# Performance work log

Hardware: AMD Instinct MI355X
Metric: run time of the kernel (lower is better)

The kernel has to match this reference:

```python
import jax, jax.numpy as jnp
import numpy as np

B_LARGE, B_SMALL = 256, 256
R_LARGE, R_SMALL = 64, 16
N_LARGE, N_SMALL = 128, 128
D = 4096


def setup_inputs() -> dict:
    key = jax.random.key(0)
    k1, k2, k3, k4, k5 = jax.random.split(key, 5)
    x = jax.random.normal(k1, (B_LARGE + B_SMALL, 1, D), dtype=jnp.float16)
    wids_large = jax.random.randint(k2, (B_LARGE,), 0, N_LARGE, dtype=jnp.int32)
    wids_small = jax.random.randint(k3, (B_SMALL,), 0, N_SMALL, dtype=jnp.int32)
    lora_A_large = (jax.random.normal(k4, (N_LARGE, D, R_LARGE), dtype=jnp.float16) * jnp.float16(0.02))
    lora_A_small = (jax.random.normal(k5, (N_SMALL, D, R_SMALL), dtype=jnp.float16) * jnp.float16(0.02))
    return {"x": x, "wids_large": wids_large, "wids_small": wids_small,
            "lora_A_large": lora_A_large, "lora_A_small": lora_A_small}


def reference(x, wids_large, wids_small, lora_A_large, lora_A_small):
    # split batch into large / small adapter groups
    x_l = x[:B_LARGE]          # [Bl, 1, D]
    x_s = x[B_LARGE:]          # [Bs, 1, D]
    # gather per-sample adapter matrices, then batched matmul (BGMV pattern)
    A_l = lora_A_large[wids_large]   # [Bl, D, r_large]
    A_s = lora_A_small[wids_small]   # [Bs, D, r_small]
    y_large = jnp.einsum('bsd,bdr->bsr', x_l, A_l)  # [Bl, 1, r_large]
    y_small = jnp.einsum('bsd,bdr->bsr', x_s, A_s)  # [Bs, 1, r_small]
    return (y_large, y_small)
```

## Files before the change

### kernel.cpp

```cpp
#include <hip/hip_runtime.h>

#define NDIM 4096
#define B_LG 256
#define B_SM 256
#define N_WID 128
#define R_LG 64
#define R_SM 16
#define BLOCK 512
#define MAXB 256
#define PF 8
#define OUT_SIZE (B_LG * R_LG + B_SM * R_SM)

typedef float floatv4 __attribute__((ext_vector_type(4)));

#define WS_CNT_L 0
#define WS_CNT_S 128
#define WS_BKT_L 256
#define WS_BKT_S (256 + N_WID * MAXB)

__global__ __launch_bounds__(BLOCK)
void setup_kernel(const int* __restrict__ wids_l,
                  const int* __restrict__ wids_s,
                  int* __restrict__ ws,
                  float* __restrict__ out)
{
    __shared__ int cl[N_WID], cs[N_WID];
    const int t = threadIdx.x;
    if (t < N_WID) { cl[t] = 0; cs[t] = 0; }
    __syncthreads();
    if (t < B_LG) {
        const int w = wids_l[t];
        const int s = atomicAdd(&cl[w], 1);
        ws[WS_BKT_L + w * MAXB + s] = t;
    } else if (t < B_LG + B_SM) {
        const int b = t - B_LG;
        const int w = wids_s[b];
        const int s = atomicAdd(&cs[w], 1);
        ws[WS_BKT_S + w * MAXB + s] = b;
    }
    __syncthreads();
    if (t < N_WID) { ws[WS_CNT_L + t] = cl[t]; ws[WS_CNT_S + t] = cs[t]; }
    for (int i = t; i < OUT_SIZE; i += BLOCK) out[i] = 0.0f;
}

template<int R, int M, int DCH>
__device__ __forceinline__ void gemv_chunk(
    const float* __restrict__ x,
    const float* __restrict__ Ab,
    float* __restrict__ outb,
    const int* __restrict__ batches,
    int d0,
    float* __restrict__ xs,
    float* __restrict__ red)
{
    constexpr int LPR  = R / 4;
    constexpr int ROWS = BLOCK / LPR;
    constexpr int IT   = DCH / ROWS;
    constexpr int NG   = IT / PF;

    const int t = threadIdx.x;

    int rows[M];
#pragma unroll
    for (int m = 0; m < M; ++m) rows[m] = batches[m];

    __syncthreads();
#pragma unroll
    for (int m = 0; m < M; ++m)
        for (int i = t; i < DCH / 4; i += BLOCK)
            reinterpret_cast<float4*>(xs + m * DCH)[i] =
                reinterpret_cast<const float4*>(x + (size_t)rows[m] * NDIM + d0)[i];
    __syncthreads();

    const int d_sub  = t / LPR;
    const int r_base = (t % LPR) * 4;
    const float* Abt = Ab + ((size_t)d0 + d_sub) * R + r_base;

    float acc[M][4];
#pragma unroll
    for (int m = 0; m < M; ++m)
#pragma unroll
        for (int j = 0; j < 4; ++j) acc[m][j] = 0.0f;

#pragma unroll
    for (int g = 0; g < NG; ++g) {
        floatv4 buf[PF];
#pragma unroll
        for (int p = 0; p < PF; ++p)
            buf[p] = __builtin_nontemporal_load(
                reinterpret_cast<const floatv4*>(Abt + (size_t)(g * PF + p) * ROWS * R));
#pragma unroll
        for (int p = 0; p < PF; ++p) {
            const int d = (g * PF + p) * ROWS + d_sub;
#pragma unroll
            for (int m = 0; m < M; ++m) {
                const float xv = xs[m * DCH + d];
                acc[m][0] = fmaf(xv, buf[p].x, acc[m][0]);
                acc[m][1] = fmaf(xv, buf[p].y, acc[m][1]);
                acc[m][2] = fmaf(xv, buf[p].z, acc[m][2]);
                acc[m][3] = fmaf(xv, buf[p].w, acc[m][3]);
            }
        }
    }

    const int wave = t >> 6;
    const int lane = t & 63;
#pragma unroll
    for (int m = 0; m < M; ++m)
#pragma unroll
        for (int off = 32; off >= LPR; off >>= 1)
#pragma unroll
            for (int j = 0; j < 4; ++j)
                acc[m][j] += __shfl_down(acc[m][j], off, 64);

#pragma unroll
    for (int m = 0; m < M; ++m) {
        __syncthreads();
        if (lane < LPR)
#pragma unroll
            for (int j = 0; j < 4; ++j) red[(wave * 16 + lane) * 4 + j] = acc[m][j];
        __syncthreads();
        if (t < R) {
            const int rl = t / 4, j = t % 4;
            float v = 0.0f;
#pragma unroll
            for (int w = 0; w < 8; ++w) v += red[(w * 16 + rl) * 4 + j];
            atomicAdd(outb + (size_t)rows[m] * R + t, v);
        }
    }
}

template<int R, int DCH, int MAXM>
__device__ __forceinline__ void run_wid_chunk(
    const float* x, const float* Ab, float* outb,
    const int* bucket, int count, int d0,
    float* xs, float* red)
{
    for (int g = 0; g < count; g += MAXM) {
        const int Mi = min(MAXM, count - g);
        const int* b = bucket + g;
        if (Mi == 1)      gemv_chunk<R, 1, DCH>(x, Ab, outb, b, d0, xs, red);
        else if (Mi == 2) gemv_chunk<R, 2, DCH>(x, Ab, outb, b, d0, xs, red);
        else if (Mi == 3) gemv_chunk<R, 3, DCH>(x, Ab, outb, b, d0, xs, red);
        else {
            if constexpr (MAXM > 3) {
                if (Mi == 4)      gemv_chunk<R, 4, DCH>(x, Ab, outb, b, d0, xs, red);
                else if (Mi == 5) gemv_chunk<R, 5, DCH>(x, Ab, outb, b, d0, xs, red);
                else              gemv_chunk<R, 6, DCH>(x, Ab, outb, b, d0, xs, red);
            }
        }
    }
}

__global__ __launch_bounds__(BLOCK, 4)
void SequentialLoraA_kernel(const float* __restrict__ x,
                            const float* __restrict__ Al,
                            const float* __restrict__ As,
                            float* __restrict__ out,
                            const int* __restrict__ ws)
{
    __shared__ float xs[6 * 1024];
    __shared__ float red[8 * 16 * 4];

    const int blk = blockIdx.x;
    if (blk < 4 * N_WID) {
        const int wid = blk >> 2;
        const int d0  = (blk & 3) * 1024;
        run_wid_chunk<R_LG, 1024, 6>(x,
                                     Al + (size_t)wid * NDIM * R_LG,
                                     out,
                                     ws + WS_BKT_L + wid * MAXB,
                                     ws[WS_CNT_L + wid], d0,
                                     xs, red);
    } else {
        const int b2  = blk - 4 * N_WID;
        const int wid = b2 >> 1;
        const int d0  = (b2 & 1) * 2048;
        run_wid_chunk<R_SM, 2048, 3>(x + (size_t)B_LG * NDIM,
                                     As + (size_t)wid * NDIM * R_SM,
                                     out + (size_t)B_LG * R_LG,
                                     ws + WS_BKT_S + wid * MAXB,
                                     ws[WS_CNT_S + wid], d0,
                                     xs, red);
    }
}

extern "C" void kernel_launch(void* const* d_in, const int* in_sizes, int n_in,
                              void* d_out, int out_size, void* d_ws, size_t ws_size,
                              hipStream_t stream) {
    const float* x      = (const float*)d_in[0];
    const int*   wids_l = (const int*)d_in[1];
    const int*   wids_s = (const int*)d_in[2];
    const float* Al     = (const float*)d_in[3];
    const float* As     = (const float*)d_in[4];
    float* out = (float*)d_out;
    int*   ws  = (int*)d_ws;

    setup_kernel<<<1, BLOCK, 0, stream>>>(wids_l, wids_s, ws, out);
    SequentialLoraA_kernel<<<6 * N_WID, BLOCK, 0, stream>>>(x, Al, As, out, ws);
}
```

Baseline: 223.7 us.

## Replace static per-adapter grid with dynamic work queue over finer D-chunks

The setup kernel now builds a flat list of work items, one per (adapter, group of up to 6 samples, D-chunk), and the main kernel pulls items from it through an atomic ticket in a persistent-style loop over 1024 blocks. D-chunks shrink (512 for large rank, 1024 for small rank), so there are more, smaller items and less imbalance from adapters that have many samples. The cost is one atomic per item, extra barriers, more atomicAdd partial-sum traffic on the output, and some repeated reads of x.

```diff
diff --git a/kernel.cpp b/kernel.cpp
--- a/kernel.cpp
+++ b/kernel.cpp
@@ -8,15 +8,25 @@
 #define R_SM 16
 #define BLOCK 512
 #define MAXB 256
+#define MAXM 6
 #define PF 8
 #define OUT_SIZE (B_LG * R_LG + B_SM * R_SM)
 
+#define DCH_LG 512
+#define DCH_SM 1024
+#define NCH_LG (NDIM / DCH_LG)
+#define NCH_SM (NDIM / DCH_SM)
+
 typedef float floatv4 __attribute__((ext_vector_type(4)));
 
-#define WS_CNT_L 0
-#define WS_CNT_S 128
-#define WS_BKT_L 256
-#define WS_BKT_S (256 + N_WID * MAXB)
+#define WS_CNT_L  0
+#define WS_CNT_S  128
+#define WS_NWORK  256
+#define WS_TICKET 260
+#define WS_BKT_L  512
+#define WS_BKT_S  (WS_BKT_L + N_WID * MAXB)
+#define WS_WORK   (WS_BKT_S + N_WID * MAXB)
+#define MAX_WORK  4096
 
 __global__ __launch_bounds__(BLOCK)
 void setup_kernel(const int* __restrict__ wids_l,
@@ -25,8 +35,10 @@
                   float* __restrict__ out)
 {
     __shared__ int cl[N_WID], cs[N_WID];
+    __shared__ int nwork;
     const int t = threadIdx.x;
     if (t < N_WID) { cl[t] = 0; cs[t] = 0; }
+    if (t == 0) nwork = 0;
     __syncthreads();
     if (t < B_LG) {
         const int w = wids_l[t];
@@ -39,7 +51,30 @@
         ws[WS_BKT_S + w * MAXB + s] = b;
     }
     __syncthreads();
-    if (t < N_WID) { ws[WS_CNT_L + t] = cl[t]; ws[WS_CNT_S + t] = cs[t]; }
+    if (t < N_WID) {
+        ws[WS_CNT_L + t] = cl[t];
+        ws[WS_CNT_S + t] = cs[t];
+        int cnt = cl[t];
+        for (int g = 0; g < cnt; g += MAXM) {
+            const int Mi   = min(MAXM, cnt - g);
+            const int base = atomicAdd(&nwork, NCH_LG);
+            for (int c = 0; c < NCH_LG; ++c) {
+                ws[WS_WORK + 2 * (base + c)]     = (t << 8) | c;
+                ws[WS_WORK + 2 * (base + c) + 1] = (g << 8) | Mi;
+            }
+        }
+        cnt = cs[t];
+        for (int g = 0; g < cnt; g += MAXM) {
+            const int Mi   = min(MAXM, cnt - g);
+            const int base = atomicAdd(&nwork, NCH_SM);
+            for (int c = 0; c < NCH_SM; ++c) {
+                ws[WS_WORK + 2 * (base + c)]     = (1 << 30) | (t << 8) | c;
+                ws[WS_WORK + 2 * (base + c) + 1] = (g << 8) | Mi;
+            }
+        }
+    }
+    __syncthreads();
+    if (t == 0) { ws[WS_NWORK] = nwork; ws[WS_TICKET] = 0; }
     for (int i = t; i < OUT_SIZE; i += BLOCK) out[i] = 0.0f;
 }
 
@@ -64,7 +99,6 @@
 #pragma unroll
     for (int m = 0; m < M; ++m) rows[m] = batches[m];
 
-    __syncthreads();
 #pragma unroll
     for (int m = 0; m < M; ++m)
         for (int i = t; i < DCH / 4; i += BLOCK)
@@ -130,58 +164,60 @@
     }
 }
 
-template<int R, int DCH, int MAXM>
-__device__ __forceinline__ void run_wid_chunk(
-    const float* x, const float* Ab, float* outb,
-    const int* bucket, int count, int d0,
-    float* xs, float* red)
-{
-    for (int g = 0; g < count; g += MAXM) {
-        const int Mi = min(MAXM, count - g);
-        const int* b = bucket + g;
-        if (Mi == 1)      gemv_chunk<R, 1, DCH>(x, Ab, outb, b, d0, xs, red);
-        else if (Mi == 2) gemv_chunk<R, 2, DCH>(x, Ab, outb, b, d0, xs, red);
-        else if (Mi == 3) gemv_chunk<R, 3, DCH>(x, Ab, outb, b, d0, xs, red);
-        else {
-            if constexpr (MAXM > 3) {
-                if (Mi == 4)      gemv_chunk<R, 4, DCH>(x, Ab, outb, b, d0, xs, red);
-                else if (Mi == 5) gemv_chunk<R, 5, DCH>(x, Ab, outb, b, d0, xs, red);
-                else              gemv_chunk<R, 6, DCH>(x, Ab, outb, b, d0, xs, red);
-            }
-        }
-    }
-}
-
 __global__ __launch_bounds__(BLOCK, 4)
 void SequentialLoraA_kernel(const float* __restrict__ x,
                             const float* __restrict__ Al,
                             const float* __restrict__ As,
                             float* __restrict__ out,
-                            const int* __restrict__ ws)
+                            int* __restrict__ ws)
 {
-    __shared__ float xs[6 * 1024];
+    __shared__ float xs[MAXM * DCH_SM];
     __shared__ float red[8 * 16 * 4];
-
-    const int blk = blockIdx.x;
-    if (blk < 4 * N_WID) {
-        const int wid = blk >> 2;
-        const int d0  = (blk & 3) * 1024;
-        run_wid_chunk<R_LG, 1024, 6>(x,
-                                     Al + (size_t)wid * NDIM * R_LG,
-                                     out,
-                                     ws + WS_BKT_L + wid * MAXB,
-                                     ws[WS_CNT_L + wid], d0,
-                                     xs, red);
-    } else {
-        const int b2  = blk - 4 * N_WID;
-        const int wid = b2 >> 1;
-        const int d0  = (b2 & 1) * 2048;
-        run_wid_chunk<R_SM, 2048, 3>(x + (size_t)B_LG * NDIM,
-                                     As + (size_t)wid * NDIM * R_SM,
-                                     out + (size_t)B_LG * R_LG,
-                                     ws + WS_BKT_S + wid * MAXB,
-                                     ws[WS_CNT_S + wid], d0,
-                                     xs, red);
+    __shared__ int s_item;
+
+    const int t  = threadIdx.x;
+    const int nw = ws[WS_NWORK];
+
+    for (;;) {
+        __syncthreads();
+        if (t == 0) s_item = atomicAdd(ws + WS_TICKET, 1);
+        __syncthreads();
+        const int it = s_item;
+        if (it >= nw) return;
+
+        const int a   = ws[WS_WORK + 2 * it];
+        const int b   = ws[WS_WORK + 2 * it + 1];
+        const int wid = (a >> 8) & 0x7f;
+        const int Mi  = b & 0xff;
+        const int gs  = b >> 8;
+
+        if (a & (1 << 30)) {
+            const int d0 = (a & 0xff) * DCH_SM;
+            const float* xb  = x + (size_t)B_LG * NDIM;
+            const float* Ab  = As + (size_t)wid * NDIM * R_SM;
+            float*       ob  = out + (size_t)B_LG * R_LG;
+            const int*   bkt = ws + WS_BKT_S + wid * MAXB + gs;
+            switch (Mi) {
+              case 1: gemv_chunk<R_SM, 1, DCH_SM>(xb, Ab, ob, bkt, d0, xs, red); break;
+              case 2: gemv_chunk<R_SM, 2, DCH_SM>(xb, Ab, ob, bkt, d0, xs, red); break;
+              case 3: gemv_chunk<R_SM, 3, DCH_SM>(xb, Ab, ob, bkt, d0, xs, red); break;
+              case 4: gemv_chunk<R_SM, 4, DCH_SM>(xb, Ab, ob, bkt, d0, xs, red); break;
+              case 5: gemv_chunk<R_SM, 5, DCH_SM>(xb, Ab, ob, bkt, d0, xs, red); break;
+              default: gemv_chunk<R_SM, 6, DCH_SM>(xb, Ab, ob, bkt, d0, xs, red); break;
+            }
+        } else {
+            const int d0 = (a & 0xff) * DCH_LG;
+            const float* Ab  = Al + (size_t)wid * NDIM * R_LG;
+            const int*   bkt = ws + WS_BKT_L + wid * MAXB + gs;
+            switch (Mi) {
+              case 1: gemv_chunk<R_LG, 1, DCH_LG>(x, Ab, out, bkt, d0, xs, red); break;
+              case 2: gemv_chunk<R_LG, 2, DCH_LG>(x, Ab, out, bkt, d0, xs, red); break;
+              case 3: gemv_chunk<R_LG, 3, DCH_LG>(x, Ab, out, bkt, d0, xs, red); break;
+              case 4: gemv_chunk<R_LG, 4, DCH_LG>(x, Ab, out, bkt, d0, xs, red); break;
+              case 5: gemv_chunk<R_LG, 5, DCH_LG>(x, Ab, out, bkt, d0, xs, red); break;
+              default: gemv_chunk<R_LG, 6, DCH_LG>(x, Ab, out, bkt, d0, xs, red); break;
+            }
+        }
     }
 }
 
@@ -197,5 +233,5 @@
     int*   ws  = (int*)d_ws;
 
     setup_kernel<<<1, BLOCK, 0, stream>>>(wids_l, wids_s, ws, out);
-    SequentialLoraA_kernel<<<6 * N_WID, BLOCK, 0, stream>>>(x, Al, As, out, ws);
-}
+    SequentialLoraA_kernel<<<1024, BLOCK, 0, stream>>>(x, Al, As, out, ws);
+}
```

After: 228.5 us. 1.02x slower.
